# Optimization experiments

Measured on AMD Instinct MI355X. Metric: run time of the kernel, lower is better.

## Reference

```python
import jax, jax.numpy as jnp
from jax import lax
import numpy as np

MAX_ITER = 12      # sifting iterations per IMF
TOL = 0.05         # sd tolerance / flatness tolerance
NUM_IMFS = 6       # max IMFs extracted
EPS = 1e-8


def _peak_mask(s):
    # strict local maxima, matching scipy.signal.find_peaks on plateau-free
    # (continuous random) signals: s[i-1] < s[i] > s[i+1]
    interior = (s[:, 1:-1] > s[:, :-2]) & (s[:, 1:-1] > s[:, 2:])
    return jnp.pad(interior, ((0, 0), (1, 1)))  # [B, L] bool


def _interp_env(s, mask):
    # piecewise-linear interpolation through masked peaks, flat extrapolation
    # at the ends (np.interp with left=first peak val, right=last peak val)
    B, L = s.shape
    idx = jnp.arange(L)
    last = lax.cummax(jnp.where(mask, idx, -1), axis=1)               # prev peak idx (-1 if none)
    nxt = lax.cummin(jnp.where(mask, idx, L), axis=1, reverse=True)   # next peak idx (L if none)
    vl = jnp.take_along_axis(s, jnp.clip(last, 0, L - 1), axis=1)
    vr = jnp.take_along_axis(s, jnp.clip(nxt, 0, L - 1), axis=1)
    denom = nxt - last
    frac = jnp.where(denom > 0,
                     (idx - last).astype(s.dtype) / jnp.maximum(denom, 1).astype(s.dtype),
                     jnp.zeros((), s.dtype))
    env = vl + frac * (vr - vl)
    env = jnp.where(last < 0, vr, env)   # left of first peak
    env = jnp.where(nxt >= L, vl, env)   # right of last peak
    return env


def _envelope(s, upper):
    mask = _peak_mask(s) if upper else _peak_mask(-s)
    env = _interp_env(s, mask)
    # fallback when fewer than 2 peaks: running max / running min of s
    fb = lax.cummax(s, axis=1) if upper else lax.cummin(s, axis=1)
    few = mask.sum(axis=1, keepdims=True) < 2
    return jnp.where(few, fb, env)


def _extract_imf(signal):
    # iterative sifting with early-stop masked into a fixed-length scan
    def body(carry, _):
        h, done = carry
        mean = 0.5 * (_envelope(h, True) + _envelope(h, False))
        # sd = sum((h - h_new)^2) / (sum(h^2)+eps) and h - h_new == mean
        sd = jnp.sum(mean ** 2) / (jnp.sum(h ** 2) + EPS)
        conv = sd < TOL
        h_next = jnp.where(done | conv, h, h - mean)
        return (h_next, done | conv), None
    (h, _), _ = lax.scan(body, (signal, jnp.array(False)), None, length=MAX_ITER)
    return h, signal - h


def _emd(x):
    def step(carry, _):
        res, done = carry
        imf, new_res = _extract_imf(res)
        imf = jnp.where(done, jnp.zeros_like(imf), imf)
        new_res = jnp.where(done, res, new_res)
        # _is_residual_flat: var(diff) < tol * var(residual) (torch.var unbiased)
        d = jnp.diff(new_res, axis=-1)
        flat = jnp.var(d, ddof=1) < TOL * jnp.var(new_res, ddof=1)
        return (new_res, done | flat), imf
    (res, _), imfs = lax.scan(step, (x, jnp.array(False)), None, length=NUM_IMFS)
    # stack IMFs and residual: [NUM_IMFS+1, B, L]; IMFs after early stop are zeros
    return jnp.concatenate([imfs, res[None]], axis=0)


def setup_inputs() -> dict:
    key = jax.random.key(0)
    x = jax.random.normal(key, (64, 16384), dtype=jnp.float32)
    return {"x": x}


def reference(x):
    return _emd(x)
```

## Files before the change

### kernel.cpp

```cpp
#include <hip/hip_runtime.h>

#define NL 16384
#define NB 64
#define NT 512
#define NC (NL / NT)
#define NW (NT / 64)
#define N_ITER 12
#define N_IMFS 6

#pragma clang fp contract(off)

#define HSZ (NL + (NL >> 5))
__device__ __forceinline__ int physi(int i) { return i + (i >> 5); }

#define FMAXV 3.402823466e38f

__global__ __launch_bounds__(NT, 2) void emd_main(
    const float* __restrict__ x, float* __restrict__ out,
    unsigned* cnt, double* sdsl, double* flsl) {
  __shared__ float h[HSZ];
  __shared__ float meanb[HSZ];
  __shared__ int wLU[NW], wLL[NW], wNU[NW], wNL[NW];
  __shared__ float wMx[NW], wMn[NW];
  __shared__ unsigned wCT[NW];
  __shared__ int eLU[NW], eLL[NW], eNU[NW], eNL[NW];
  __shared__ float eMx[NW], eMn[NW];
  __shared__ unsigned sTot;
  __shared__ double tA[NW], tB[NW], tC[NW], tD[NW];
  __shared__ int sFlag;

  const int t = threadIdx.x;
  const int lane = t & 63;
  const int wv = t >> 6;
  const int row = blockIdx.x;
  const int base = t * NC;
  const float* xr = x + (size_t)row * NL;
  float* res = out + (size_t)N_IMFS * NB * NL + (size_t)row * NL;

  for (int m = 0; m < NC; m++) {
    int i = m * NT + t;
    float v = xr[i];
    h[physi(i)] = v;
    res[i] = v;
  }
  __syncthreads();

  unsigned ep = 0;
  bool done = false;

  for (int k = 0; k < N_IMFS; k++) {
    float* outk = out + (size_t)k * NB * NL + (size_t)row * NL;
    if (done) {
      for (int m = 0; m < NC; m++) outk[m * NT + t] = 0.0f;
      continue;
    }

    for (int it = 0; it < N_ITER; it++) {
      unsigned mU = 0, mL = 0;
      int lmU = -1, lmL = -1, cU = 0, cL = 0;
      float rmx = -FMAXV, rmn = FMAXV;
      {
        float hm = (base > 0) ? h[physi(base - 1)] : 0.0f;
        float hc = h[physi(base)];
        #pragma unroll
        for (int j = 0; j < NC; j++) {
          int i = base + j;
          float hp = (i + 1 < NL) ? h[physi(i + 1)] : 0.0f;
          bool in = (i > 0) && (i + 1 < NL);
          if (in && hm < hc && hc > hp) { mU |= (1u << j); lmU = i; cU++; }
          if (in && hm > hc && hc < hp) { mL |= (1u << j); lmL = i; cL++; }
          rmx = fmaxf(rmx, hc);
          rmn = fminf(rmn, hc);
          hm = hc; hc = hp;
        }
      }
      int iLU = lmU, iLL = lmL;
      float iMx = rmx, iMn = rmn;
      int iNU = mU ? (base + __ffs(mU) - 1) : NL;
      int iNL = mL ? (base + __ffs(mL) - 1) : NL;
      unsigned ict = ((unsigned)cU << 16) | (unsigned)cL;
      #pragma unroll
      for (int o = 1; o < 64; o <<= 1) {
        int a = __shfl_up(iLU, o, 64);
        int b = __shfl_up(iLL, o, 64);
        float fa = __shfl_up(iMx, o, 64);
        float fb = __shfl_up(iMn, o, 64);
        int c = __shfl_down(iNU, o, 64);
        int d = __shfl_down(iNL, o, 64);
        unsigned cc = __shfl_down(ict, o, 64);
        if (lane >= o) { iLU = max(iLU, a); iLL = max(iLL, b);
                         iMx = fmaxf(iMx, fa); iMn = fminf(iMn, fb); }
        if (lane + o < 64) { iNU = min(iNU, c); iNL = min(iNL, d); ict += cc; }
      }
      if (lane == 63) { wLU[wv] = iLU; wLL[wv] = iLL; wMx[wv] = iMx; wMn[wv] = iMn; }
      if (lane == 0)  { wNU[wv] = iNU; wNL[wv] = iNL; wCT[wv] = ict; }
      __syncthreads();
      if (t == 0) {
        int aLU = -1, aLL = -1; float aMx = -FMAXV, aMn = FMAXV; unsigned tot = 0;
        for (int w = 0; w < NW; w++) {
          eLU[w] = aLU; aLU = max(aLU, wLU[w]);
          eLL[w] = aLL; aLL = max(aLL, wLL[w]);
          eMx[w] = aMx; aMx = fmaxf(aMx, wMx[w]);
          eMn[w] = aMn; aMn = fminf(aMn, wMn[w]);
          tot += wCT[w];
        }
        int aNU = NL, aNL = NL;
        for (int w = NW - 1; w >= 0; w--) {
          eNU[w] = aNU; aNU = min(aNU, wNU[w]);
          eNL[w] = aNL; aNL = min(aNL, wNL[w]);
        }
        sTot = tot;
      }
      __syncthreads();
      unsigned tot = sTot;
      int totU = (int)(tot >> 16), totL = (int)(tot & 0xffffu);
      int pLU = __shfl_up(iLU, 1, 64); if (lane == 0) pLU = -1;
      int pLL = __shfl_up(iLL, 1, 64); if (lane == 0) pLL = -1;
      float pMx = __shfl_up(iMx, 1, 64); if (lane == 0) pMx = -FMAXV;
      float pMn = __shfl_up(iMn, 1, 64); if (lane == 0) pMn = FMAXV;
      int sNUl = __shfl_down(iNU, 1, 64); if (lane == 63) sNUl = NL;
      int sNLl = __shfl_down(iNL, 1, 64); if (lane == 63) sNLl = NL;
      const int clU = max(eLU[wv], pLU), clL = max(eLL[wv], pLL);
      const float crx = fmaxf(eMx[wv], pMx), crn = fminf(eMn[wv], pMn);
      const int cnU = min(eNU[wv], sNUl), cnL = min(eNL[wv], sNLl);

      double pm2 = 0.0, ph2 = 0.0;
      {
        float rx = crx, rn = crn;
        int gA = -0x7fffffff, gB = -0x7fffffff, gC = -0x7fffffff, gD = -0x7fffffff;
        float vl = 0.0f, vr = 0.0f, wl = 0.0f, wr = 0.0f;
        #pragma unroll
        for (int j = 0; j < NC; j++) {
          int i = base + j;
          float hc = h[physi(i)];
          rx = fmaxf(rx, hc);
          rn = fminf(rn, hc);
          unsigned lowm = 0xFFFFFFFFu >> (31 - j);
          unsigned highm = 0xFFFFFFFFu << j;
          unsigned a;
          a = mU & lowm;  int lU  = a ? (base + 31 - __clz(a)) : clU;
          a = mL & lowm;  int lL  = a ? (base + 31 - __clz(a)) : clL;
          a = mU & highm; int nUv = a ? (base + __ffs(a) - 1) : cnU;
          a = mL & highm; int nLv = a ? (base + __ffs(a) - 1) : cnL;
          if (lU != gA)  { gA = lU;  vl = h[physi(lU < 0 ? 0 : lU)]; }
          if (nUv != gB) { gB = nUv; vr = h[physi(nUv >= NL ? NL - 1 : nUv)]; }
          if (lL != gC)  { gC = lL;  wl = h[physi(lL < 0 ? 0 : lL)]; }
          if (nLv != gD) { gD = nLv; wr = h[physi(nLv >= NL ? NL - 1 : nLv)]; }
          int den = nUv - lU;
          float fracU = (float)(i - lU) / (float)(den > 0 ? den : 1);
          float envU = (den > 0) ? __builtin_fmaf(fracU, vr - vl, vl) : vl;
          if (lU < 0) envU = vr;
          if (nUv >= NL) envU = vl;
          if (totU < 2) envU = rx;
          int den2 = nLv - lL;
          float fracL = (float)(i - lL) / (float)(den2 > 0 ? den2 : 1);
          float envL = (den2 > 0) ? __builtin_fmaf(fracL, wr - wl, wl) : wl;
          if (lL < 0) envL = wr;
          if (nLv >= NL) envL = wl;
          if (totL < 2) envL = rn;
          float mn = 0.5f * (envU + envL);
          meanb[physi(i)] = mn;
          pm2 += (double)mn * (double)mn;
          ph2 += (double)hc * (double)hc;
        }
      }
      #pragma unroll
      for (int o = 1; o < 64; o <<= 1) {
        double a = __shfl_down(pm2, o, 64);
        double b = __shfl_down(ph2, o, 64);
        if (lane + o < 64) { pm2 += a; ph2 += b; }
      }
      if (lane == 0) { tA[wv] = pm2; tB[wv] = ph2; }
      ep++;
      __syncthreads();
      if (t == 0) {
        double sA = 0.0, sB = 0.0;
        for (int w = 0; w < NW; w++) { sA += tA[w]; sB += tB[w]; }
        atomicAdd(&sdsl[(k * N_ITER + it) * 2 + 0], sA);
        atomicAdd(&sdsl[(k * N_ITER + it) * 2 + 1], sB);
        __hip_atomic_fetch_add(cnt, 1u, __ATOMIC_ACQ_REL, __HIP_MEMORY_SCOPE_AGENT);
        unsigned tgt = ep * gridDim.x;
        while (__hip_atomic_load(cnt, __ATOMIC_ACQUIRE, __HIP_MEMORY_SCOPE_AGENT) < tgt)
          __builtin_amdgcn_s_sleep(1);
        double m2 = __hip_atomic_load(&sdsl[(k * N_ITER + it) * 2 + 0],
                                      __ATOMIC_RELAXED, __HIP_MEMORY_SCOPE_AGENT);
        double h2 = __hip_atomic_load(&sdsl[(k * N_ITER + it) * 2 + 1],
                                      __ATOMIC_RELAXED, __HIP_MEMORY_SCOPE_AGENT);
        sFlag = (m2 / (h2 + 1e-8) < 0.05) ? 1 : 0;
      }
      __syncthreads();
      if (sFlag) break;
      #pragma unroll
      for (int q = 0; q < NC / 4; q++) {
        int p0 = physi(base + q * 4);
        float4 hv = *(const float4*)&h[p0];
        float4 mv = *(const float4*)&meanb[p0];
        hv.x -= mv.x; hv.y -= mv.y; hv.z -= mv.z; hv.w -= mv.w;
        *(float4*)&h[p0] = hv;
      }
      __syncthreads();
    }

    double s1 = 0.0, s2 = 0.0, s3 = 0.0, s4 = 0.0;
    {
      float rc = res[base] - h[physi(base)];
      #pragma unroll
      for (int j = 0; j < NC; j++) {
        int i = base + j;
        s1 += (double)rc;
        s2 += (double)rc * (double)rc;
        if (i + 1 < NL) {
          float rnx = res[i + 1] - h[physi(i + 1)];
          float d = rnx - rc;
          s3 += (double)d;
          s4 += (double)d * (double)d;
          rc = rnx;
        }
      }
    }
    #pragma unroll
    for (int o = 1; o < 64; o <<= 1) {
      double a = __shfl_down(s1, o, 64);
      double b = __shfl_down(s2, o, 64);
      double c = __shfl_down(s3, o, 64);
      double d = __shfl_down(s4, o, 64);
      if (lane + o < 64) { s1 += a; s2 += b; s3 += c; s4 += d; }
    }
    if (lane == 0) { tA[wv] = s1; tB[wv] = s2; tC[wv] = s3; tD[wv] = s4; }
    __syncthreads();
    if (t == 0) {
      double S1 = 0.0, S2 = 0.0, S3 = 0.0, S4 = 0.0;
      for (int w = 0; w < NW; w++) { S1 += tA[w]; S2 += tB[w]; S3 += tC[w]; S4 += tD[w]; }
      atomicAdd(&flsl[k * 4 + 0], S1);
      atomicAdd(&flsl[k * 4 + 1], S2);
      atomicAdd(&flsl[k * 4 + 2], S3);
      atomicAdd(&flsl[k * 4 + 3], S4);
    }
    #pragma unroll
    for (int q = 0; q < NC / 4; q++) {
      int i0 = base + q * 4;
      int p0 = physi(i0);
      float4 rv = *(const float4*)&res[i0];
      float4 hv = *(const float4*)&h[p0];
      float4 rq = make_float4(rv.x - hv.x, rv.y - hv.y, rv.z - hv.z, rv.w - hv.w);
      *(float4*)&outk[i0] = hv;
      *(float4*)&res[i0] = rq;
      *(float4*)&h[p0] = rq;
    }
    ep++;
    __syncthreads();
    if (t == 0) {
      __hip_atomic_fetch_add(cnt, 1u, __ATOMIC_ACQ_REL, __HIP_MEMORY_SCOPE_AGENT);
      unsigned tgt = ep * gridDim.x;
      while (__hip_atomic_load(cnt, __ATOMIC_ACQUIRE, __HIP_MEMORY_SCOPE_AGENT) < tgt)
        __builtin_amdgcn_s_sleep(1);
      double S1 = __hip_atomic_load(&flsl[k * 4 + 0], __ATOMIC_RELAXED, __HIP_MEMORY_SCOPE_AGENT);
      double S2 = __hip_atomic_load(&flsl[k * 4 + 1], __ATOMIC_RELAXED, __HIP_MEMORY_SCOPE_AGENT);
      double S3 = __hip_atomic_load(&flsl[k * 4 + 2], __ATOMIC_RELAXED, __HIP_MEMORY_SCOPE_AGENT);
      double S4 = __hip_atomic_load(&flsl[k * 4 + 3], __ATOMIC_RELAXED, __HIP_MEMORY_SCOPE_AGENT);
      double nr = (double)NB * (double)NL;
      double nd = (double)NB * (double)(NL - 1);
      double varr = (S2 - S1 * S1 / nr) / (nr - 1.0);
      double vard = (S4 - S3 * S3 / nd) / (nd - 1.0);
      sFlag = (vard < 0.05 * varr) ? 1 : 0;
    }
    __syncthreads();
    done = done || (sFlag != 0);
  }
}

extern "C" void kernel_launch(void* const* d_in, const int* in_sizes, int n_in,
                              void* d_out, int out_size, void* d_ws, size_t ws_size,
                              hipStream_t stream) {
  const float* x = (const float*)d_in[0];
  float* out = (float*)d_out;
  size_t zb = ws_size < 4096 ? ws_size : 4096;
  hipMemsetAsync(d_ws, 0, zb, stream);
  unsigned* cnt = (unsigned*)d_ws;
  double* sdsl = (double*)((char*)d_ws + 256);
  double* flsl = (double*)((char*)d_ws + 256 + (size_t)N_IMFS * N_ITER * 2 * 8);
  hipLaunchKernelGGL(emd_main, dim3(NB), dim3(NT), 0, stream, x, out, cnt, sdsl, flsl);
}
```

Before: 330.3 us.

## Overlap grid-wide sd barrier with next iteration using a dedicated sync wave

Adds a ninth wavefront that only handles the cross-block sd reduction and spin-wait, so the data waves apply h -= mean speculatively and start the next peak scan while the grid barrier resolves. If the previous iteration turns out converged, h is restored from the saved copy kept in meanb. This takes the global barrier latency off the critical path of each sifting iteration. In exchange the block grows to 576 threads with launch bounds occupancy 1, and every converged iteration does one extra, wasted scan.

Measured after the change: 343.8 us. 1.04x slower.

```diff
diff --git a/kernel.cpp b/kernel.cpp
--- a/kernel.cpp
+++ b/kernel.cpp
@@ -2,9 +2,10 @@
 
 #define NL 16384
 #define NB 64
-#define NT 512
-#define NC (NL / NT)
-#define NW (NT / 64)
+#define NDT 512
+#define NT  576
+#define NC (NL / NDT)
+#define NW (NDT / 64)
 #define N_ITER 12
 #define N_IMFS 6
 
@@ -15,7 +16,7 @@
 
 #define FMAXV 3.402823466e38f
 
-__global__ __launch_bounds__(NT, 2) void emd_main(
+__global__ __launch_bounds__(NT, 1) void emd_main(
     const float* __restrict__ x, float* __restrict__ out,
     unsigned* cnt, double* sdsl, double* flsl) {
   __shared__ float h[HSZ];
@@ -32,16 +33,19 @@
   const int t = threadIdx.x;
   const int lane = t & 63;
   const int wv = t >> 6;
+  const bool dataT = (t < NDT);
   const int row = blockIdx.x;
   const int base = t * NC;
   const float* xr = x + (size_t)row * NL;
   float* res = out + (size_t)N_IMFS * NB * NL + (size_t)row * NL;
 
-  for (int m = 0; m < NC; m++) {
-    int i = m * NT + t;
-    float v = xr[i];
-    h[physi(i)] = v;
-    res[i] = v;
+  if (dataT) {
+    for (int m = 0; m < NC; m++) {
+      int i = m * NDT + t;
+      float v = xr[i];
+      h[physi(i)] = v;
+      res[i] = v;
+    }
   }
   __syncthreads();
 
@@ -51,15 +55,19 @@
   for (int k = 0; k < N_IMFS; k++) {
     float* outk = out + (size_t)k * NB * NL + (size_t)row * NL;
     if (done) {
-      for (int m = 0; m < NC; m++) outk[m * NT + t] = 0.0f;
+      if (dataT) for (int m = 0; m < NC; m++) outk[m * NDT + t] = 0.0f;
       continue;
     }
 
-    for (int it = 0; it < N_ITER; it++) {
-      unsigned mU = 0, mL = 0;
-      int lmU = -1, lmL = -1, cU = 0, cL = 0;
-      float rmx = -FMAXV, rmn = FMAXV;
-      {
+    unsigned mU = 0, mL = 0;
+    int iLU = -1, iLL = -1, iNU = NL, iNL = NL;
+    float iMx = -FMAXV, iMn = FMAXV;
+
+    for (int it = 0; it <= N_ITER; it++) {
+      if (dataT) {
+        mU = 0; mL = 0;
+        int lmU = -1, lmL = -1, cU = 0, cL = 0;
+        float rmx = -FMAXV, rmn = FMAXV;
         float hm = (base > 0) ? h[physi(base - 1)] : 0.0f;
         float hc = h[physi(base)];
         #pragma unroll
@@ -73,27 +81,36 @@
           rmn = fminf(rmn, hc);
           hm = hc; hc = hp;
         }
-      }
-      int iLU = lmU, iLL = lmL;
-      float iMx = rmx, iMn = rmn;
-      int iNU = mU ? (base + __ffs(mU) - 1) : NL;
-      int iNL = mL ? (base + __ffs(mL) - 1) : NL;
-      unsigned ict = ((unsigned)cU << 16) | (unsigned)cL;
-      #pragma unroll
-      for (int o = 1; o < 64; o <<= 1) {
-        int a = __shfl_up(iLU, o, 64);
-        int b = __shfl_up(iLL, o, 64);
-        float fa = __shfl_up(iMx, o, 64);
-        float fb = __shfl_up(iMn, o, 64);
-        int c = __shfl_down(iNU, o, 64);
-        int d = __shfl_down(iNL, o, 64);
-        unsigned cc = __shfl_down(ict, o, 64);
-        if (lane >= o) { iLU = max(iLU, a); iLL = max(iLL, b);
-                         iMx = fmaxf(iMx, fa); iMn = fminf(iMn, fb); }
-        if (lane + o < 64) { iNU = min(iNU, c); iNL = min(iNL, d); ict += cc; }
-      }
-      if (lane == 63) { wLU[wv] = iLU; wLL[wv] = iLL; wMx[wv] = iMx; wMn[wv] = iMn; }
-      if (lane == 0)  { wNU[wv] = iNU; wNL[wv] = iNL; wCT[wv] = ict; }
+        iLU = lmU; iLL = lmL; iMx = rmx; iMn = rmn;
+        iNU = mU ? (base + __ffs(mU) - 1) : NL;
+        iNL = mL ? (base + __ffs(mL) - 1) : NL;
+        unsigned ict = ((unsigned)cU << 16) | (unsigned)cL;
+        #pragma unroll
+        for (int o = 1; o < 64; o <<= 1) {
+          int a = __shfl_up(iLU, o, 64);
+          int b = __shfl_up(iLL, o, 64);
+          float fa = __shfl_up(iMx, o, 64);
+          float fb = __shfl_up(iMn, o, 64);
+          int c = __shfl_down(iNU, o, 64);
+          int d = __shfl_down(iNL, o, 64);
+          unsigned cc = __shfl_down(ict, o, 64);
+          if (lane >= o) { iLU = max(iLU, a); iLL = max(iLL, b);
+                           iMx = fmaxf(iMx, fa); iMn = fminf(iMn, fb); }
+          if (lane + o < 64) { iNU = min(iNU, c); iNL = min(iNL, d); ict += cc; }
+        }
+        if (lane == 63) { wLU[wv] = iLU; wLL[wv] = iLL; wMx[wv] = iMx; wMn[wv] = iMn; }
+        if (lane == 0)  { wNU[wv] = iNU; wNL[wv] = iNL; wCT[wv] = ict; }
+      } else if (t == NDT && it > 0) {
+        unsigned tgt = ep * gridDim.x;
+        while (__hip_atomic_load(cnt, __ATOMIC_ACQUIRE, __HIP_MEMORY_SCOPE_AGENT) < tgt)
+          __builtin_amdgcn_s_sleep(1);
+        int slot = k * N_ITER + (it - 1);
+        double m2 = __hip_atomic_load(&sdsl[slot * 2 + 0],
+                                      __ATOMIC_RELAXED, __HIP_MEMORY_SCOPE_AGENT);
+        double h2 = __hip_atomic_load(&sdsl[slot * 2 + 1],
+                                      __ATOMIC_RELAXED, __HIP_MEMORY_SCOPE_AGENT);
+        sFlag = (m2 / (h2 + 1e-8) < 0.05) ? 1 : 0;
+      }
       __syncthreads();
       if (t == 0) {
         int aLU = -1, aLL = -1; float aMx = -FMAXV, aMn = FMAXV; unsigned tot = 0;
@@ -112,20 +129,38 @@
         sTot = tot;
       }
       __syncthreads();
-      unsigned tot = sTot;
-      int totU = (int)(tot >> 16), totL = (int)(tot & 0xffffu);
-      int pLU = __shfl_up(iLU, 1, 64); if (lane == 0) pLU = -1;
-      int pLL = __shfl_up(iLL, 1, 64); if (lane == 0) pLL = -1;
-      float pMx = __shfl_up(iMx, 1, 64); if (lane == 0) pMx = -FMAXV;
-      float pMn = __shfl_up(iMn, 1, 64); if (lane == 0) pMn = FMAXV;
-      int sNUl = __shfl_down(iNU, 1, 64); if (lane == 63) sNUl = NL;
-      int sNLl = __shfl_down(iNL, 1, 64); if (lane == 63) sNLl = NL;
-      const int clU = max(eLU[wv], pLU), clL = max(eLL[wv], pLL);
-      const float crx = fmaxf(eMx[wv], pMx), crn = fminf(eMn[wv], pMn);
-      const int cnU = min(eNU[wv], sNUl), cnL = min(eNL[wv], sNLl);
+
+      if (it > 0 && sFlag) {
+        if (dataT) {
+          #pragma unroll
+          for (int q = 0; q < NC / 4; q++) {
+            int p0 = physi(base + q * 4);
+            *(float4*)&h[p0] = *(const float4*)&meanb[p0];
+          }
+        }
+        __syncthreads();
+        break;
+      }
+      if (it == N_ITER) break;
+
+      int clU = 0, clL = 0, cnU = 0, cnL = 0, totU = 0, totL = 0;
+      float crx = 0.0f, crn = 0.0f;
+      if (dataT) {
+        unsigned tot = sTot;
+        totU = (int)(tot >> 16); totL = (int)(tot & 0xffffu);
+        int pLU = __shfl_up(iLU, 1, 64); if (lane == 0) pLU = -1;
+        int pLL = __shfl_up(iLL, 1, 64); if (lane == 0) pLL = -1;
+        float pMx = __shfl_up(iMx, 1, 64); if (lane == 0) pMx = -FMAXV;
+        float pMn = __shfl_up(iMn, 1, 64); if (lane == 0) pMn = FMAXV;
+        int sNUl = __shfl_down(iNU, 1, 64); if (lane == 63) sNUl = NL;
+        int sNLl = __shfl_down(iNL, 1, 64); if (lane == 63) sNLl = NL;
+        clU = max(eLU[wv], pLU); clL = max(eLL[wv], pLL);
+        crx = fmaxf(eMx[wv], pMx); crn = fminf(eMn[wv], pMn);
+        cnU = min(eNU[wv], sNUl); cnL = min(eNL[wv], sNLl);
+      }
 
       double pm2 = 0.0, ph2 = 0.0;
-      {
+      if (dataT) {
         float rx = crx, rn = crn;
         int gA = -0x7fffffff, gB = -0x7fffffff, gC = -0x7fffffff, gD = -0x7fffffff;
         float vl = 0.0f, vr = 0.0f, wl = 0.0f, wr = 0.0f;
@@ -163,46 +198,39 @@
           pm2 += (double)mn * (double)mn;
           ph2 += (double)hc * (double)hc;
         }
-      }
-      #pragma unroll
-      for (int o = 1; o < 64; o <<= 1) {
-        double a = __shfl_down(pm2, o, 64);
-        double b = __shfl_down(ph2, o, 64);
-        if (lane + o < 64) { pm2 += a; ph2 += b; }
-      }
-      if (lane == 0) { tA[wv] = pm2; tB[wv] = ph2; }
+        #pragma unroll
+        for (int o = 1; o < 64; o <<= 1) {
+          double a2 = __shfl_down(pm2, o, 64);
+          double b2 = __shfl_down(ph2, o, 64);
+          if (lane + o < 64) { pm2 += a2; ph2 += b2; }
+        }
+        if (lane == 0) { tA[wv] = pm2; tB[wv] = ph2; }
+      }
       ep++;
       __syncthreads();
-      if (t == 0) {
+      if (dataT) {
+        #pragma unroll
+        for (int q = 0; q < NC / 4; q++) {
+          int p0 = physi(base + q * 4);
+          float4 hv = *(const float4*)&h[p0];
+          float4 mv = *(const float4*)&meanb[p0];
+          float4 nh = make_float4(hv.x - mv.x, hv.y - mv.y, hv.z - mv.z, hv.w - mv.w);
+          *(float4*)&h[p0] = nh;
+          *(float4*)&meanb[p0] = hv;
+        }
+      } else if (t == NDT) {
         double sA = 0.0, sB = 0.0;
         for (int w = 0; w < NW; w++) { sA += tA[w]; sB += tB[w]; }
-        atomicAdd(&sdsl[(k * N_ITER + it) * 2 + 0], sA);
-        atomicAdd(&sdsl[(k * N_ITER + it) * 2 + 1], sB);
+        int slot = k * N_ITER + it;
+        atomicAdd(&sdsl[slot * 2 + 0], sA);
+        atomicAdd(&sdsl[slot * 2 + 1], sB);
         __hip_atomic_fetch_add(cnt, 1u, __ATOMIC_ACQ_REL, __HIP_MEMORY_SCOPE_AGENT);
-        unsigned tgt = ep * gridDim.x;
-        while (__hip_atomic_load(cnt, __ATOMIC_ACQUIRE, __HIP_MEMORY_SCOPE_AGENT) < tgt)
-          __builtin_amdgcn_s_sleep(1);
-        double m2 = __hip_atomic_load(&sdsl[(k * N_ITER + it) * 2 + 0],
-                                      __ATOMIC_RELAXED, __HIP_MEMORY_SCOPE_AGENT);
-        double h2 = __hip_atomic_load(&sdsl[(k * N_ITER + it) * 2 + 1],
-                                      __ATOMIC_RELAXED, __HIP_MEMORY_SCOPE_AGENT);
-        sFlag = (m2 / (h2 + 1e-8) < 0.05) ? 1 : 0;
       }
       __syncthreads();
-      if (sFlag) break;
-      #pragma unroll
-      for (int q = 0; q < NC / 4; q++) {
-        int p0 = physi(base + q * 4);
-        float4 hv = *(const float4*)&h[p0];
-        float4 mv = *(const float4*)&meanb[p0];
-        hv.x -= mv.x; hv.y -= mv.y; hv.z -= mv.z; hv.w -= mv.w;
-        *(float4*)&h[p0] = hv;
-      }
-      __syncthreads();
     }
 
     double s1 = 0.0, s2 = 0.0, s3 = 0.0, s4 = 0.0;
-    {
+    if (dataT) {
       float rc = res[base] - h[physi(base)];
       #pragma unroll
       for (int j = 0; j < NC; j++) {
@@ -217,16 +245,16 @@
           rc = rnx;
         }
       }
-    }
-    #pragma unroll
-    for (int o = 1; o < 64; o <<= 1) {
-      double a = __shfl_down(s1, o, 64);
-      double b = __shfl_down(s2, o, 64);
-      double c = __shfl_down(s3, o, 64);
-      double d = __shfl_down(s4, o, 64);
-      if (lane + o < 64) { s1 += a; s2 += b; s3 += c; s4 += d; }
-    }
-    if (lane == 0) { tA[wv] = s1; tB[wv] = s2; tC[wv] = s3; tD[wv] = s4; }
+      #pragma unroll
+      for (int o = 1; o < 64; o <<= 1) {
+        double a = __shfl_down(s1, o, 64);
+        double b = __shfl_down(s2, o, 64);
+        double c = __shfl_down(s3, o, 64);
+        double d = __shfl_down(s4, o, 64);
+        if (lane + o < 64) { s1 += a; s2 += b; s3 += c; s4 += d; }
+      }
+      if (lane == 0) { tA[wv] = s1; tB[wv] = s2; tC[wv] = s3; tD[wv] = s4; }
+    }
     __syncthreads();
     if (t == 0) {
       double S1 = 0.0, S2 = 0.0, S3 = 0.0, S4 = 0.0;
@@ -236,16 +264,18 @@
       atomicAdd(&flsl[k * 4 + 2], S3);
       atomicAdd(&flsl[k * 4 + 3], S4);
     }
-    #pragma unroll
-    for (int q = 0; q < NC / 4; q++) {
-      int i0 = base + q * 4;
-      int p0 = physi(i0);
-      float4 rv = *(const float4*)&res[i0];
-      float4 hv = *(const float4*)&h[p0];
-      float4 rq = make_float4(rv.x - hv.x, rv.y - hv.y, rv.z - hv.z, rv.w - hv.w);
-      *(float4*)&outk[i0] = hv;
-      *(float4*)&res[i0] = rq;
-      *(float4*)&h[p0] = rq;
+    if (dataT) {
+      #pragma unroll
+      for (int q = 0; q < NC / 4; q++) {
+        int i0 = base + q * 4;
+        int p0 = physi(i0);
+        float4 rv = *(const float4*)&res[i0];
+        float4 hv = *(const float4*)&h[p0];
+        float4 rq = make_float4(rv.x - hv.x, rv.y - hv.y, rv.z - hv.z, rv.w - hv.w);
+        *(float4*)&outk[i0] = hv;
+        *(float4*)&res[i0] = rq;
+        *(float4*)&h[p0] = rq;
+      }
     }
     ep++;
     __syncthreads();
```
